# Kernel tuning notes

Measured on AMD Instinct MI355X. Metric: run time of the kernel, lower is better.

## Reference

```python
import jax, jax.numpy as jnp
from jax import lax
import numpy as np

HEADS = 8
DIM_HEAD = 64


def setup_inputs() -> dict:
    key = jax.random.key(0)
    ks = jax.random.split(key, 6)
    dim, inner = 256, HEADS * DIM_HEAD
    fmap = jax.random.normal(ks[0], (8, dim, 128, 128), dtype=jnp.float32)
    w_q = jax.random.normal(ks[1], (inner, dim), dtype=jnp.float32) * (dim ** -0.5)
    w_dw = jax.random.normal(ks[2], (dim, 1, 3, 3), dtype=jnp.float32) * (9 ** -0.5)
    w_pw = jax.random.normal(ks[3], (2 * inner, dim), dtype=jnp.float32) * (dim ** -0.5)
    w_out = jax.random.normal(ks[4], (dim, inner), dtype=jnp.float32) * (inner ** -0.5)
    b_out = jnp.zeros((dim,), dtype=jnp.float32)
    return {"fmap": fmap, "w_q": w_q, "w_dw": w_dw, "w_pw": w_pw, "w_out": w_out, "b_out": b_out}


def _linear_attention(fmap, w_q, w_dw, w_pw, w_out, b_out):
    B, C, H, W = fmap.shape
    h, d = HEADS, DIM_HEAD
    scale = d ** -0.5
    N = H * W
    # to_q: 1x1 conv, no bias
    q = jnp.einsum('bcxy,oc->boxy', fmap, w_q)  # [B, h*d, H, W]
    # to_kv: depthwise 3x3 (pad 1) then pointwise 1x1, no bias
    dw = lax.conv_general_dilated(
        fmap, w_dw, window_strides=(1, 1), padding=((1, 1), (1, 1)),
        dimension_numbers=('NCHW', 'OIHW', 'NCHW'), feature_group_count=C)
    kv = jnp.einsum('bcxy,oc->boxy', dw, w_pw)  # [B, 2*h*d, H, W]
    k, v = jnp.split(kv, 2, axis=1)

    def to_bhnc(t):  # b (h c) x y -> (b h) (x y) c
        return t.reshape(B, h, d, N).transpose(0, 1, 3, 2).reshape(B * h, N, d)

    q, k, v = to_bhnc(q), to_bhnc(k), to_bhnc(v)
    q = jax.nn.softmax(q, axis=-1) * scale  # softmax over feature dim
    k = jax.nn.softmax(k, axis=-2)          # softmax over spatial dim
    context = jnp.einsum('bnd,bne->bde', k, v)   # [(B*h), d, d]
    out = jnp.einsum('bnd,bde->bne', q, context)  # [(B*h), N, d]
    # (b h) (x y) d -> b (h d) x y
    out = out.reshape(B, h, N, d).transpose(0, 1, 3, 2).reshape(B, h * d, H, W)
    out = jax.nn.gelu(out, approximate=False)
    out = jnp.einsum('bcxy,oc->boxy', out, w_out) + b_out[None, :, None, None]
    return out


def reference(fmap, w_q, w_dw, w_pw, w_out, b_out):
    return _linear_attention(fmap, w_q, w_dw, w_pw, w_out, b_out)
```

## Files before the change

kernel.cpp:

```cpp
#include <hip/hip_runtime.h>
#include <math.h>

#define NPIX 16384

typedef __bf16 bf16x8 __attribute__((ext_vector_type(8)));
typedef float f32x4 __attribute__((ext_vector_type(4)));
typedef unsigned short u16;
typedef unsigned int u32;

__device__ __forceinline__ u16 f2bf(float f) {
    u32 u = __float_as_uint(f);
    u32 r = (u + 0x7FFFu + ((u >> 16) & 1u)) >> 16;
    return (u16)r;
}
__device__ __forceinline__ float bf2f(u32 s) { return __uint_as_float(s << 16); }
__device__ __forceinline__ u32 pk2(float a, float b) {
    return (u32)f2bf(a) | ((u32)f2bf(b) << 16);
}

__global__ __launch_bounds__(256) void k_cvtw(
    const float* __restrict__ wq, const float* __restrict__ wpw,
    const float* __restrict__ wout,
    u16* __restrict__ wq_b, u16* __restrict__ wpw_b, u16* __restrict__ wout_b)
{
    int id = (blockIdx.x * 256 + threadIdx.x) * 4;
    const float* s; u16* d; int off;
    if (id < 131072)      { s = wq;   d = wq_b;   off = id; }
    else if (id < 393216) { s = wpw;  d = wpw_b;  off = id - 131072; }
    else                  { s = wout; d = wout_b; off = id - 393216; }
    f32x4 v = *(const f32x4*)(s + off);
    uint2 u; u.x = pk2(v[0], v[1]); u.y = pk2(v[2], v[3]);
    *(uint2*)(d + off) = u;
}

__global__ __launch_bounds__(256) void k_conv(
    const float* __restrict__ fmap, const float* __restrict__ wdw,
    u16* __restrict__ fmapT, u16* __restrict__ dwT)
{
    const int t = threadIdx.x;
    const int lane = t & 63, w = t >> 6;
    const int x = blockIdx.x, b = blockIdx.y;

    __shared__ u16 dst[2][128][66];

    const float mLf = (lane == 0) ? 0.f : 1.f;
    const float mRf = (lane == 63) ? 0.f : 1.f;
    const float mTf = (x > 0) ? 1.f : 0.f;
    const float mBf = (x < 127) ? 1.f : 0.f;
    const int dT = (x > 0) ? -128 : 0;
    const int dB = (x < 127) ? 128 : 0;

    const size_t nbase = (size_t)b * NPIX + (size_t)x * 128;

    for (int chunk = 0; chunk < 4; ++chunk) {
        for (int g = 0; g < 4; ++g) {
            const int cl0 = w * 16 + g * 4;
            const int c0 = chunk * 64 + cl0;
            float2 T[4], M[4], B[4];
            #pragma unroll
            for (int i = 0; i < 4; ++i) {
                const float* p = fmap + ((size_t)(b * 256 + c0 + i)) * NPIX + (size_t)x * 128;
                M[i] = ((const float2*)p)[lane];
                T[i] = ((const float2*)(p + dT))[lane];
                B[i] = ((const float2*)(p + dB))[lane];
            }
            #pragma unroll
            for (int i = 0; i < 4; ++i) {
                const float* wc = wdw + (c0 + i) * 9;
                float w0 = wc[0] * mTf, w1 = wc[1] * mTf, w2 = wc[2] * mTf;
                float w3 = wc[3],       w4 = wc[4],       w5 = wc[5];
                float w6 = wc[6] * mBf, w7 = wc[7] * mBf, w8 = wc[8] * mBf;
                float tL = __shfl_up(T[i].y, 1) * mLf;
                float mL_ = __shfl_up(M[i].y, 1) * mLf;
                float bL = __shfl_up(B[i].y, 1) * mLf;
                float tR = __shfl_down(T[i].x, 1) * mRf;
                float mR_ = __shfl_down(M[i].x, 1) * mRf;
                float bR = __shfl_down(B[i].x, 1) * mRf;
                float o0 = w0 * tL     + w1 * T[i].x + w2 * T[i].y
                         + w3 * mL_    + w4 * M[i].x + w5 * M[i].y
                         + w6 * bL     + w7 * B[i].x + w8 * B[i].y;
                float o1 = w0 * T[i].x + w1 * T[i].y + w2 * tR
                         + w3 * M[i].x + w4 * M[i].y + w5 * mR_
                         + w6 * B[i].x + w7 * B[i].y + w8 * bR;
                int cl = cl0 + i;
                dst[0][2 * lane][cl]     = f2bf(M[i].x);
                dst[0][2 * lane + 1][cl] = f2bf(M[i].y);
                dst[1][2 * lane][cl]     = f2bf(o0);
                dst[1][2 * lane + 1][cl] = f2bf(o1);
            }
        }
        __syncthreads();
        #pragma unroll
        for (int T2 = 0; T2 < 2; ++T2) {
            u16* gp = T2 ? dwT : fmapT;
            #pragma unroll
            for (int it = 0; it < 4; ++it) {
                int u = it * 256 + t;
                int y = u >> 3, c8 = (u & 7) * 8;
                const u16* s = &dst[T2][y][c8];
                uint4 val;
                val.x = *(const u32*)(s);
                val.y = *(const u32*)(s + 2);
                val.z = *(const u32*)(s + 4);
                val.w = *(const u32*)(s + 6);
                *(uint4*)(gp + (nbase + y) * 256 + chunk * 64 + c8) = val;
            }
        }
        __syncthreads();
    }
}

__global__ __launch_bounds__(256, 2) void k_kvctx(
    const u16* __restrict__ dwT, const u16* __restrict__ wpw,
    float* __restrict__ ctx, float* __restrict__ denom)
{
    const int t = threadIdx.x;
    const int lane = t & 63, w = t >> 6;
    const int l15 = lane & 15, quad = lane >> 4;

    const int L = blockIdx.x;
    const int work = (L & 7) * 128 + (L >> 3);
    const int s = work >> 6;
    const int b = (work >> 3) & 7;
    const int h = work & 7;
    const int bh = b * 8 + h;

    __shared__ __align__(16) u16 sm[32768];
    u16* EL = sm;
    u16* VL = sm + 8192;

    const int ph = (w & 1) * 64;
    const int ck = (w >> 1);

    const int srow = t >> 3;
    const int sg = t & 7;

    f32x4 ctxacc[4] = {};
    float dpart[4] = {0.f, 0.f, 0.f, 0.f};

    uint4 ra[4], rb[4];

#define KV_STAGE_LOAD(stv, kcv)                                                        \
    {                                                                                  \
        const u16* xr = dwT + ((size_t)b * NPIX + s * 1024 + (stv) * 128) * 256;       \
        _Pragma("unroll")                                                              \
        for (int p = 0; p < 4; ++p) {                                                  \
            int row = srow + 32 * p;                                                   \
            int wr = (row < 64) ? (h * 64 + row) : (512 + h * 64 + (row - 64));        \
            ra[p] = *(const uint4*)(wpw + (size_t)wr * 256 + (kcv) * 64 + sg * 8);     \
            rb[p] = *(const uint4*)(xr + (size_t)row * 256 + (kcv) * 64 + sg * 8);     \
        }                                                                              \
    }

#define KV_STAGE_WRITE(bufi)                                                           \
    {                                                                                  \
        u16* Ad = sm + (bufi) * 8192;                                                  \
        u16* Bd = sm + 16384 + (bufi) * 8192;                                          \
        _Pragma("unroll")                                                              \
        for (int p = 0; p < 4; ++p) {                                                  \
            int row = srow + 32 * p;                                                   \
            int off = row * 64 + ((sg ^ (row & 7)) << 3);                              \
            *(uint4*)(Ad + off) = ra[p];                                               \
            *(uint4*)(Bd + off) = rb[p];                                               \
        }                                                                              \
    }

    KV_STAGE_LOAD(0, 0);

    for (int st = 0; st < 8; ++st) {
        KV_STAGE_WRITE(0);
        __syncthreads();
        f32x4 acc[4][4] = {};
        #pragma unroll
        for (int kc = 0; kc < 4; ++kc) {
            if (kc < 3) KV_STAGE_LOAD(st, kc + 1);
            {
                const u16* Ax = sm + (kc & 1) * 8192;
                const u16* Bx = sm + 16384 + (kc & 1) * 8192;
                #pragma unroll
                for (int kk = 0; kk < 64; kk += 32) {
                    bf16x8 av[4], bv[4];
                    #pragma unroll
                    for (int mf = 0; mf < 4; ++mf) {
                        int pr = ph + mf * 16 + l15;
                        int pg = ((kk >> 3) + quad) ^ (pr & 7);
                        av[mf] = *(const bf16x8*)(Bx + pr * 64 + (pg << 3));
                    }
                    #pragma unroll
                    for (int nf = 0; nf < 4; ++nf) {
                        int wr2 = ck * 64 + nf * 16 + l15;
                        int wg = ((kk >> 3) + quad) ^ (wr2 & 7);
                        bv[nf] = *(const bf16x8*)(Ax + wr2 * 64 + (wg << 3));
                    }
                    #pragma unroll
                    for (int mf = 0; mf < 4; ++mf)
                        #pragma unroll
                        for (int nf = 0; nf < 4; ++nf)
                            acc[mf][nf] = __builtin_amdgcn_mfma_f32_16x16x32_bf16(av[mf], bv[nf], acc[mf][nf], 0, 0, 0);
                }
            }
            if (kc < 3) {
                KV_STAGE_WRITE((kc + 1) & 1);
                __syncthreads();
            }
        }
        __syncthreads();
        u16* dst = ck ? VL : EL;
        #pragma unroll
        for (int nf = 0; nf < 4; ++nf) {
            const int ch = nf * 16 + l15;
            const int key = ch & 7;
            float colsum = 0.f;
            #pragma unroll
            for (int mf = 0; mf < 4; ++mf) {
                const int c = ph + mf * 16 + quad * 4;
                float v0 = acc[mf][nf][0], v1 = acc[mf][nf][1];
                float v2 = acc[mf][nf][2], v3 = acc[mf][nf][3];
                if (ck == 0) {
                    v0 = __expf(v0); v1 = __expf(v1);
                    v2 = __expf(v2); v3 = __expf(v3);
                    colsum += (v0 + v1) + (v2 + v3);
                }
                uint2 u; u.x = pk2(v0, v1); u.y = pk2(v2, v3);
                int addr = ch * 128 + ((((c >> 3) ^ key)) << 3) + (c & 7);
                *(uint2*)(dst + addr) = u;
            }
            if (ck == 0) {
                colsum += __shfl_xor(colsum, 16);
                colsum += __shfl_xor(colsum, 32);
                dpart[nf] += colsum;
            }
        }
        if (st < 7) KV_STAGE_LOAD(st + 1, 0);
        __syncthreads();
        #pragma unroll
        for (int kk2 = 0; kk2 < 128; kk2 += 32) {
            int ar = w * 16 + l15;
            int ag = ((kk2 >> 3) + quad) ^ (ar & 7);
            bf16x8 av = *(const bf16x8*)(VL + ar * 128 + (ag << 3));
            #pragma unroll
            for (int nf = 0; nf < 4; ++nf) {
                int br = nf * 16 + l15;
                int bg = ((kk2 >> 3) + quad) ^ (br & 7);
                bf16x8 bv = *(const bf16x8*)(EL + br * 128 + (bg << 3));
                ctxacc[nf] = __builtin_amdgcn_mfma_f32_16x16x32_bf16(av, bv, ctxacc[nf], 0, 0, 0);
            }
        }
        __syncthreads();
    }
    #pragma unroll
    for (int nf = 0; nf < 4; ++nf)
        #pragma unroll
        for (int r = 0; r < 4; ++r) {
            int e = w * 16 + quad * 4 + r;
            int d = nf * 16 + l15;
            atomicAdd(ctx + ((size_t)bh * 64 + e) * 64 + d, ctxacc[nf][r]);
        }
    if (ck == 0 && quad == 0) {
        #pragma unroll
        for (int nf = 0; nf < 4; ++nf)
            atomicAdd(denom + bh * 64 + nf * 16 + l15, dpart[nf]);
    }
#undef KV_STAGE_LOAD
#undef KV_STAGE_WRITE
}

__global__ __launch_bounds__(256) void k_proj_q(
    const u16* __restrict__ fmapT, const u16* __restrict__ wq,
    u16* __restrict__ q)
{
    const int t = threadIdx.x;
    const int lane = t & 63, w = t >> 6;
    const int l15 = lane & 15, quad = lane >> 4;
    const int n0 = blockIdx.x * 128;
    const int o0 = blockIdx.y * 128;
    const int b  = blockIdx.z;
    __shared__ __align__(16) unsigned char smraw[71680];
    u16* sm16 = (u16*)smraw;
    f32x4 acc[4][4] = {};
    const int mh = (w >> 1) * 64, nh = (w & 1) * 64;
    const u16* wrow = wq + (size_t)o0 * 256;
    const u16* xrow = fmapT + ((size_t)b * NPIX + n0) * 256;
    const int srow = t >> 3;
    const int sg = t & 7;
    uint4 ra[4], rb[4];

#define Q_STAGE_LOAD(kcv)                                                              \
    {                                                                                  \
        _Pragma("unroll")                                                              \
        for (int p = 0; p < 4; ++p) {                                                  \
            int row = srow + 32 * p;                                                   \
            ra[p] = *(const uint4*)(wrow + (size_t)row * 256 + (kcv) * 64 + sg * 8);   \
            rb[p] = *(const uint4*)(xrow + (size_t)row * 256 + (kcv) * 64 + sg * 8);   \
        }                                                                              \
    }

#define Q_STAGE_WRITE(bufi)                                                            \
    {                                                                                  \
        u16* Ad = sm16 + (bufi) * 8192;                                                \
        u16* Bd = sm16 + 16384 + (bufi) * 8192;                                        \
        _Pragma("unroll")                                                              \
        for (int p = 0; p < 4; ++p) {                                                  \
            int row = srow + 32 * p;                                                   \
            int off = row * 64 + ((sg ^ (row & 7)) << 3);                              \
            *(uint4*)(Ad + off) = ra[p];                                               \
            *(uint4*)(Bd + off) = rb[p];                                               \
        }                                                                              \
    }

    Q_STAGE_LOAD(0);
    Q_STAGE_WRITE(0);
    __syncthreads();
    #pragma unroll
    for (int kc = 0; kc < 4; ++kc) {
        if (kc < 3) Q_STAGE_LOAD(kc + 1);
        {
            const u16* Ax = sm16 + (kc & 1) * 8192;
            const u16* Bx = sm16 + 16384 + (kc & 1) * 8192;
            #pragma unroll
            for (int kk = 0; kk < 64; kk += 32) {
                bf16x8 av[4], bv[4];
                #pragma unroll
                for (int mf = 0; mf < 4; ++mf) {
                    int arow = mh + mf * 16 + l15;
                    int agr = ((kk >> 3) + quad) ^ (arow & 7);
                    av[mf] = *(const bf16x8*)(Ax + arow * 64 + (agr << 3));
                }
                #pragma unroll
                for (int nf = 0; nf < 4; ++nf) {
                    int brow = nh + nf * 16 + l15;
                    int bgr = ((kk >> 3) + quad) ^ (brow & 7);
                    bv[nf] = *(const bf16x8*)(Bx + brow * 64 + (bgr << 3));
                }
                #pragma unroll
                for (int mf = 0; mf < 4; ++mf)
                    #pragma unroll
                    for (int nf = 0; nf < 4; ++nf)
                        acc[mf][nf] = __builtin_amdgcn_mfma_f32_16x16x32_bf16(av[mf], bv[nf], acc[mf][nf], 0, 0, 0);
            }
        }
        if (kc < 3) {
            Q_STAGE_WRITE((kc + 1) & 1);
            __syncthreads();
        }
    }
    __syncthreads();
    float* ep = (float*)smraw;
    #pragma unroll
    for (int mf = 0; mf < 4; ++mf)
        #pragma unroll
        for (int nf = 0; nf < 4; ++nf)
            #pragma unroll
            for (int r = 0; r < 4; ++r) {
                int row = mh + mf * 16 + quad * 4 + r;
                int col = nh + nf * 16 + l15;
                ep[col * 140 + row] = acc[mf][nf][r];
            }
    __syncthreads();
    const int h0 = blockIdx.y * 2;
    for (int p = 0; p < 8; ++p) {
        int unit = p * 32 + (t >> 3);
        int pix = unit >> 1, hh = unit & 1;
        int d8 = (t & 7) * 8;
        f32x4 v0 = *(const f32x4*)(ep + pix * 140 + hh * 64 + d8);
        f32x4 v1 = *(const f32x4*)(ep + pix * 140 + hh * 64 + d8 + 4);
        float e0 = __expf(v0[0]), e1 = __expf(v0[1]), e2 = __expf(v0[2]), e3 = __expf(v0[3]);
        float e4 = __expf(v1[0]), e5 = __expf(v1[1]), e6 = __expf(v1[2]), e7 = __expf(v1[3]);
        float s = ((e0 + e1) + (e2 + e3)) + ((e4 + e5) + (e6 + e7));
        s += __shfl_xor(s, 1); s += __shfl_xor(s, 2); s += __shfl_xor(s, 4);
        float r = 0.125f / s;
        uint4 u;
        u.x = pk2(e0 * r, e1 * r); u.y = pk2(e2 * r, e3 * r);
        u.z = pk2(e4 * r, e5 * r); u.w = pk2(e6 * r, e7 * r);
        size_t off = (((size_t)b * 8 + h0 + hh) * NPIX + n0 + pix) * 64 + d8;
        *(uint4*)(q + off) = u;
    }
#undef Q_STAGE_LOAD
#undef Q_STAGE_WRITE
}

__global__ __launch_bounds__(256) void k_attnout(
    const u16* __restrict__ q, const float* __restrict__ ctx,
    const float* __restrict__ denom, const u16* __restrict__ wout,
    const float* __restrict__ bout, float* __restrict__ out)
{
    const int t = threadIdx.x;
    const int lane = t & 63, w = t >> 6;
    const int l15 = lane & 15, quad = lane >> 4;
    const int n0 = blockIdx.x * 32;
    const int b  = blockIdx.y;
    __shared__ __align__(16) u16 tmp[32 * 520];
    __shared__ __align__(16) unsigned char R[20480];
    u16* qs = (u16*)R;
    u16* cs = (u16*)(R + 4608);
    u16* ws = (u16*)R;
    for (int h = 0; h < 8; ++h) {
        __syncthreads();
        {
            int row = t >> 3, g = t & 7;
            *(uint4*)(qs + row * 72 + g * 8) =
                *(const uint4*)(q + (((size_t)b * 8 + h) * NPIX + n0 + row) * 64 + g * 8);
        }
        const int bh = b * 8 + h;
        #pragma unroll
        for (int p = 0; p < 4; ++p) {
            int idx = p * 256 + t;
            int e = idx >> 4, dq = (idx & 15) * 4;
            f32x4 c4 = *(const f32x4*)(ctx + ((size_t)bh * 64 + e) * 64 + dq);
            f32x4 d4 = *(const f32x4*)(denom + bh * 64 + dq);
            uint2 u;
            u.x = pk2(c4[0] / d4[0], c4[1] / d4[1]);
            u.y = pk2(c4[2] / d4[2], c4[3] / d4[3]);
            *(uint2*)(cs + e * 72 + dq) = u;
        }
        __syncthreads();
        f32x4 a1[2] = {};
        #pragma unroll
        for (int kk = 0; kk < 64; kk += 32) {
            bf16x8 av = *(const bf16x8*)(qs + ((w & 1) * 16 + l15) * 72 + kk + quad * 8);
            #pragma unroll
            for (int j = 0; j < 2; ++j) {
                int nf = (w >> 1) * 2 + j;
                bf16x8 bv = *(const bf16x8*)(cs + (nf * 16 + l15) * 72 + kk + quad * 8);
                a1[j] = __builtin_amdgcn_mfma_f32_16x16x32_bf16(av, bv, a1[j], 0, 0, 0);
            }
        }
        #pragma unroll
        for (int j = 0; j < 2; ++j)
            #pragma unroll
            for (int r = 0; r < 4; ++r) {
                int pix = (w & 1) * 16 + quad * 4 + r;
                int e = ((w >> 1) * 2 + j) * 16 + l15;
                float x = a1[j][r];
                float gel = 0.5f * x * (1.0f + erff(x * 0.70710678118654752f));
                tmp[pix * 520 + h * 64 + e] = f2bf(gel);
            }
    }
    __syncthreads();
    f32x4 acc[4][2] = {};
    for (int kc = 0; kc < 16; ++kc) {
        __syncthreads();
        #pragma unroll
        for (int p = 0; p < 4; ++p) {
            int c = (t >> 2) + 64 * p, g = t & 3;
            *(uint4*)(ws + c * 40 + g * 8) = *(const uint4*)(wout + (size_t)c * 512 + kc * 32 + g * 8);
        }
        __syncthreads();
        bf16x8 av[4], bv[2];
        #pragma unroll
        for (int mf = 0; mf < 4; ++mf)
            av[mf] = *(const bf16x8*)(ws + (w * 64 + mf * 16 + l15) * 40 + quad * 8);
        #pragma unroll
        for (int nf = 0; nf < 2; ++nf)
            bv[nf] = *(const bf16x8*)(tmp + (nf * 16 + l15) * 520 + kc * 32 + quad * 8);
        #pragma unroll
        for (int mf = 0; mf < 4; ++mf)
            #pragma unroll
            for (int nf = 0; nf < 2; ++nf)
                acc[mf][nf] = __builtin_amdgcn_mfma_f32_16x16x32_bf16(av[mf], bv[nf], acc[mf][nf], 0, 0, 0);
    }
    #pragma unroll
    for (int mf = 0; mf < 4; ++mf)
        #pragma unroll
        for (int nf = 0; nf < 2; ++nf)
            #pragma unroll
            for (int r = 0; r < 4; ++r) {
                int c = w * 64 + mf * 16 + quad * 4 + r;
                int pix = nf * 16 + l15;
                out[((size_t)b * 256 + c) * NPIX + n0 + pix] = acc[mf][nf][r] + bout[c];
            }
}

extern "C" void kernel_launch(void* const* d_in, const int* in_sizes, int n_in,
                              void* d_out, int out_size, void* d_ws, size_t ws_size,
                              hipStream_t stream)
{
    const float* fmap  = (const float*)d_in[0];
    const float* w_q   = (const float*)d_in[1];
    const float* w_dw  = (const float*)d_in[2];
    const float* w_pw  = (const float*)d_in[3];
    const float* w_out = (const float*)d_in[4];
    const float* b_out = (const float*)d_in[5];
    float* out = (float*)d_out;
    char* ws = (char*)d_ws;

    u16* dwT     = (u16*)(ws);
    u16* fmapT   = (u16*)(ws + 67108864);
    u16* q       = (u16*)(ws + 134217728);
    float* ctx   = (float*)(ws + 402653184);
    float* denom = (float*)(ws + 403701760);
    u16* wq_b    = (u16*)(ws + 403718144);
    u16* wpw_b   = (u16*)(ws + 403980288);
    u16* wout_b  = (u16*)(ws + 404504576);

    hipMemsetAsync(ws + 402653184, 0, 1048576 + 16384, stream);
    k_cvtw<<<512, 256, 0, stream>>>(w_q, w_pw, w_out, wq_b, wpw_b, wout_b);
    k_conv<<<dim3(128, 8), 256, 0, stream>>>(fmap, w_dw, fmapT, dwT);
    k_kvctx<<<1024, 256, 0, stream>>>(dwT, wpw_b, ctx, denom);
    k_proj_q<<<dim3(128, 4, 8), 256, 0, stream>>>(fmapT, wq_b, q);
    k_attnout<<<dim3(512, 8), 256, 0, stream>>>(q, ctx, denom, wout_b, b_out, out);
}
```

Before: 735.3 us.

## Precompute normalized bf16 context and pipeline per-head attnout with output projection

Adds a small kernel that divides the context by the denominator once and stores it as bf16, so each attnout block no longer redoes that fp32 division per head. The attnout kernel now handles 64 pixels per block and folds the output projection into the head loop, accumulating in registers instead of staging all heads in a 32x520 shared buffer. Loads for the next head (q, context, and the matching w_out slice) are prefetched into registers while the current head's MMAs run. This costs an extra launch, more registers and more shared memory, and w_out is reloaded per head per block.

```diff
diff --git a/kernel.cpp b/kernel.cpp
--- a/kernel.cpp
+++ b/kernel.cpp
@@ -265,6 +265,27 @@
 #undef KV_STAGE_WRITE
 }
 
+__global__ __launch_bounds__(256) void k_ctxn(
+    const float* __restrict__ ctx, const float* __restrict__ denom,
+    u16* __restrict__ ctxn)
+{
+    const int bh = blockIdx.x;
+    const int t = threadIdx.x;
+    const int e = t >> 2, d0 = (t & 3) * 16;
+    const float* cr = ctx + ((size_t)bh * 64 + e) * 64 + d0;
+    const float* dr = denom + bh * 64 + d0;
+    u16* o = ctxn + ((size_t)bh * 64 + e) * 64 + d0;
+    #pragma unroll
+    for (int i = 0; i < 4; ++i) {
+        f32x4 c = *(const f32x4*)(cr + i * 4);
+        f32x4 dv = *(const f32x4*)(dr + i * 4);
+        uint2 u;
+        u.x = pk2(c[0] / dv[0], c[1] / dv[1]);
+        u.y = pk2(c[2] / dv[2], c[3] / dv[3]);
+        *(uint2*)(o + i * 4) = u;
+    }
+}
+
 __global__ __launch_bounds__(256) void k_proj_q(
     const u16* __restrict__ fmapT, const u16* __restrict__ wq,
     u16* __restrict__ q)
@@ -380,94 +401,113 @@
 }
 
 __global__ __launch_bounds__(256) void k_attnout(
-    const u16* __restrict__ q, const float* __restrict__ ctx,
-    const float* __restrict__ denom, const u16* __restrict__ wout,
-    const float* __restrict__ bout, float* __restrict__ out)
+    const u16* __restrict__ q, const u16* __restrict__ ctxn,
+    const u16* __restrict__ wout, const float* __restrict__ bout,
+    float* __restrict__ out)
 {
     const int t = threadIdx.x;
     const int lane = t & 63, w = t >> 6;
     const int l15 = lane & 15, quad = lane >> 4;
-    const int n0 = blockIdx.x * 32;
+    const int n0 = blockIdx.x * 64;
     const int b  = blockIdx.y;
-    __shared__ __align__(16) u16 tmp[32 * 520];
-    __shared__ __align__(16) unsigned char R[20480];
-    u16* qs = (u16*)R;
-    u16* cs = (u16*)(R + 4608);
-    u16* ws = (u16*)R;
+
+    __shared__ __align__(16) u16 qs[64 * 72];
+    __shared__ __align__(16) u16 cs[64 * 72];
+    __shared__ __align__(16) u16 G [64 * 72];
+    __shared__ __align__(16) u16 WS[256 * 72];
+
+    uint4 rq[2], rc[2], rw[8];
+
+    auto LOADH = [&](int h) {
+        const u16* qb = q + (((size_t)(b * 8 + h)) * NPIX + n0) * 64;
+        const u16* cb = ctxn + ((size_t)(b * 8 + h)) * 64 * 64;
+        #pragma unroll
+        for (int p = 0; p < 2; ++p) {
+            int i = p * 256 + t; int row = i >> 3, g = i & 7;
+            rq[p] = *(const uint4*)(qb + row * 64 + g * 8);
+            rc[p] = *(const uint4*)(cb + row * 64 + g * 8);
+        }
+        #pragma unroll
+        for (int p = 0; p < 8; ++p) {
+            int i = p * 256 + t; int row = i >> 3, g = i & 7;
+            rw[p] = *(const uint4*)(wout + (size_t)row * 512 + h * 64 + g * 8);
+        }
+    };
+    auto WRITEH = [&]() {
+        #pragma unroll
+        for (int p = 0; p < 2; ++p) {
+            int i = p * 256 + t; int row = i >> 3, g = i & 7;
+            *(uint4*)(qs + row * 72 + g * 8) = rq[p];
+            *(uint4*)(cs + row * 72 + g * 8) = rc[p];
+        }
+        #pragma unroll
+        for (int p = 0; p < 8; ++p) {
+            int i = p * 256 + t; int row = i >> 3, g = i & 7;
+            *(uint4*)(WS + row * 72 + g * 8) = rw[p];
+        }
+    };
+
+    f32x4 acc[4][4] = {};
+
+    LOADH(0);
+    WRITEH();
+    __syncthreads();
+
     for (int h = 0; h < 8; ++h) {
-        __syncthreads();
-        {
-            int row = t >> 3, g = t & 7;
-            *(uint4*)(qs + row * 72 + g * 8) =
-                *(const uint4*)(q + (((size_t)b * 8 + h) * NPIX + n0 + row) * 64 + g * 8);
-        }
-        const int bh = b * 8 + h;
-        #pragma unroll
-        for (int p = 0; p < 4; ++p) {
-            int idx = p * 256 + t;
-            int e = idx >> 4, dq = (idx & 15) * 4;
-            f32x4 c4 = *(const f32x4*)(ctx + ((size_t)bh * 64 + e) * 64 + dq);
-            f32x4 d4 = *(const f32x4*)(denom + bh * 64 + dq);
-            uint2 u;
-            u.x = pk2(c4[0] / d4[0], c4[1] / d4[1]);
-            u.y = pk2(c4[2] / d4[2], c4[3] / d4[3]);
-            *(uint2*)(cs + e * 72 + dq) = u;
-        }
-        __syncthreads();
-        f32x4 a1[2] = {};
+        f32x4 a1[4] = {};
         #pragma unroll
         for (int kk = 0; kk < 64; kk += 32) {
-            bf16x8 av = *(const bf16x8*)(qs + ((w & 1) * 16 + l15) * 72 + kk + quad * 8);
-            #pragma unroll
-            for (int j = 0; j < 2; ++j) {
-                int nf = (w >> 1) * 2 + j;
-                bf16x8 bv = *(const bf16x8*)(cs + (nf * 16 + l15) * 72 + kk + quad * 8);
-                a1[j] = __builtin_amdgcn_mfma_f32_16x16x32_bf16(av, bv, a1[j], 0, 0, 0);
-            }
-        }
-        #pragma unroll
-        for (int j = 0; j < 2; ++j)
-            #pragma unroll
-            for (int r = 0; r < 4; ++r) {
-                int pix = (w & 1) * 16 + quad * 4 + r;
-                int e = ((w >> 1) * 2 + j) * 16 + l15;
-                float x = a1[j][r];
-                float gel = 0.5f * x * (1.0f + erff(x * 0.70710678118654752f));
-                tmp[pix * 520 + h * 64 + e] = f2bf(gel);
-            }
-    }
-    __syncthreads();
-    f32x4 acc[4][2] = {};
-    for (int kc = 0; kc < 16; ++kc) {
-        __syncthreads();
-        #pragma unroll
-        for (int p = 0; p < 4; ++p) {
-            int c = (t >> 2) + 64 * p, g = t & 3;
-            *(uint4*)(ws + c * 40 + g * 8) = *(const uint4*)(wout + (size_t)c * 512 + kc * 32 + g * 8);
-        }
-        __syncthreads();
-        bf16x8 av[4], bv[2];
-        #pragma unroll
-        for (int mf = 0; mf < 4; ++mf)
-            av[mf] = *(const bf16x8*)(ws + (w * 64 + mf * 16 + l15) * 40 + quad * 8);
-        #pragma unroll
-        for (int nf = 0; nf < 2; ++nf)
-            bv[nf] = *(const bf16x8*)(tmp + (nf * 16 + l15) * 520 + kc * 32 + quad * 8);
-        #pragma unroll
-        for (int mf = 0; mf < 4; ++mf)
-            #pragma unroll
-            for (int nf = 0; nf < 2; ++nf)
-                acc[mf][nf] = __builtin_amdgcn_mfma_f32_16x16x32_bf16(av[mf], bv[nf], acc[mf][nf], 0, 0, 0);
+            bf16x8 av = *(const bf16x8*)(cs + (w * 16 + l15) * 72 + kk + quad * 8);
+            #pragma unroll
+            for (int nf = 0; nf < 4; ++nf) {
+                bf16x8 bv = *(const bf16x8*)(qs + (nf * 16 + l15) * 72 + kk + quad * 8);
+                a1[nf] = __builtin_amdgcn_mfma_f32_16x16x32_bf16(av, bv, a1[nf], 0, 0, 0);
+            }
+        }
+        #pragma unroll
+        for (int nf = 0; nf < 4; ++nf) {
+            int px = nf * 16 + l15;
+            int e0 = w * 16 + quad * 4;
+            float x0 = a1[nf][0], x1 = a1[nf][1], x2 = a1[nf][2], x3 = a1[nf][3];
+            x0 = 0.5f * x0 * (1.0f + erff(x0 * 0.70710678118654752f));
+            x1 = 0.5f * x1 * (1.0f + erff(x1 * 0.70710678118654752f));
+            x2 = 0.5f * x2 * (1.0f + erff(x2 * 0.70710678118654752f));
+            x3 = 0.5f * x3 * (1.0f + erff(x3 * 0.70710678118654752f));
+            uint2 u; u.x = pk2(x0, x1); u.y = pk2(x2, x3);
+            *(uint2*)(G + px * 72 + e0) = u;
+        }
+        __syncthreads();
+        if (h < 7) LOADH(h + 1);
+        #pragma unroll
+        for (int kk = 0; kk < 64; kk += 32) {
+            bf16x8 av2[4], bv2[4];
+            #pragma unroll
+            for (int mf = 0; mf < 4; ++mf)
+                av2[mf] = *(const bf16x8*)(WS + (w * 64 + mf * 16 + l15) * 72 + kk + quad * 8);
+            #pragma unroll
+            for (int nf = 0; nf < 4; ++nf)
+                bv2[nf] = *(const bf16x8*)(G + (nf * 16 + l15) * 72 + kk + quad * 8);
+            #pragma unroll
+            for (int mf = 0; mf < 4; ++mf)
+                #pragma unroll
+                for (int nf = 0; nf < 4; ++nf)
+                    acc[mf][nf] = __builtin_amdgcn_mfma_f32_16x16x32_bf16(av2[mf], bv2[nf], acc[mf][nf], 0, 0, 0);
+        }
+        __syncthreads();
+        if (h < 7) {
+            WRITEH();
+            __syncthreads();
+        }
     }
     #pragma unroll
     for (int mf = 0; mf < 4; ++mf)
         #pragma unroll
-        for (int nf = 0; nf < 2; ++nf)
+        for (int nf = 0; nf < 4; ++nf)
             #pragma unroll
             for (int r = 0; r < 4; ++r) {
                 int c = w * 64 + mf * 16 + quad * 4 + r;
-                int pix = nf * 16 + l15;
-                out[((size_t)b * 256 + c) * NPIX + n0 + pix] = acc[mf][nf][r] + bout[c];
+                int px = nf * 16 + l15;
+                out[((size_t)b * 256 + c) * NPIX + n0 + px] = acc[mf][nf][r] + bout[c];
             }
 }
 
@@ -485,6 +525,7 @@
     char* ws = (char*)d_ws;
 
     u16* dwT     = (u16*)(ws);
+    u16* ctxn    = (u16*)(ws);
     u16* fmapT   = (u16*)(ws + 67108864);
     u16* q       = (u16*)(ws + 134217728);
     float* ctx   = (float*)(ws + 402653184);
@@ -497,6 +538,7 @@
     k_cvtw<<<512, 256, 0, stream>>>(w_q, w_pw, w_out, wq_b, wpw_b, wout_b);
     k_conv<<<dim3(128, 8), 256, 0, stream>>>(fmap, w_dw, fmapT, dwT);
     k_kvctx<<<1024, 256, 0, stream>>>(dwT, wpw_b, ctx, denom);
+    k_ctxn<<<64, 256, 0, stream>>>(ctx, denom, ctxn);
     k_proj_q<<<dim3(128, 4, 8), 256, 0, stream>>>(fmapT, wq_b, q);
-    k_attnout<<<dim3(512, 8), 256, 0, stream>>>(q, ctx, denom, wout_b, b_out, out);
-}
+    k_attnout<<<dim3(256, 8), 256, 0, stream>>>(q, ctxn, wout_b, b_out, out);
+}
```

Result: slower. 842.9 us (+14.6%).

## Fuse q@context and GELU into q projection; split output projection kernel

Applied to the files above, without the earlier changes.

Context normalisation moves into a small pre-pass that writes a bf16 normalised context. The q-projection kernel then applies the feature softmax in registers and multiplies by the context with MFMA, applying GELU and writing G directly. This removes the separate q round trip and the per-block context reload in the old attention-output kernel. The output projection becomes a simpler kernel with a 128-pixel tile that reads G and w_out straight from global memory without LDS staging, which may raise register pressure and global-load traffic.

```diff
diff --git a/kernel.cpp b/kernel.cpp
--- a/kernel.cpp
+++ b/kernel.cpp
@@ -265,9 +265,30 @@
 #undef KV_STAGE_WRITE
 }
 
-__global__ __launch_bounds__(256) void k_proj_q(
+__global__ __launch_bounds__(256) void k_ctxn(
+    const float* __restrict__ ctx, const float* __restrict__ denom,
+    u16* __restrict__ ctxn)
+{
+    const int bh = blockIdx.x;
+    const int t = threadIdx.x;
+    const int e = t >> 2, d0 = (t & 3) * 16;
+    const float* cr = ctx + ((size_t)bh * 64 + e) * 64 + d0;
+    const float* dr = denom + bh * 64 + d0;
+    u16* o = ctxn + ((size_t)bh * 64 + e) * 64 + d0;
+    #pragma unroll
+    for (int i = 0; i < 4; ++i) {
+        f32x4 c = *(const f32x4*)(cr + i * 4);
+        f32x4 dv = *(const f32x4*)(dr + i * 4);
+        uint2 u;
+        u.x = pk2(c[0] / dv[0], c[1] / dv[1]);
+        u.y = pk2(c[2] / dv[2], c[3] / dv[3]);
+        *(uint2*)(o + i * 4) = u;
+    }
+}
+
+__global__ __launch_bounds__(256) void k_qattn(
     const u16* __restrict__ fmapT, const u16* __restrict__ wq,
-    u16* __restrict__ q)
+    const u16* __restrict__ ctxn, u16* __restrict__ G)
 {
     const int t = threadIdx.x;
     const int lane = t & 63, w = t >> 6;
@@ -357,118 +378,117 @@
                 ep[col * 140 + row] = acc[mf][nf][r];
             }
     __syncthreads();
-    const int h0 = blockIdx.y * 2;
-    for (int p = 0; p < 8; ++p) {
-        int unit = p * 32 + (t >> 3);
-        int pix = unit >> 1, hh = unit & 1;
-        int d8 = (t & 7) * 8;
-        f32x4 v0 = *(const f32x4*)(ep + pix * 140 + hh * 64 + d8);
-        f32x4 v1 = *(const f32x4*)(ep + pix * 140 + hh * 64 + d8 + 4);
-        float e0 = __expf(v0[0]), e1 = __expf(v0[1]), e2 = __expf(v0[2]), e3 = __expf(v0[3]);
-        float e4 = __expf(v1[0]), e5 = __expf(v1[1]), e6 = __expf(v1[2]), e7 = __expf(v1[3]);
-        float s = ((e0 + e1) + (e2 + e3)) + ((e4 + e5) + (e6 + e7));
-        s += __shfl_xor(s, 1); s += __shfl_xor(s, 2); s += __shfl_xor(s, 4);
-        float r = 0.125f / s;
-        uint4 u;
-        u.x = pk2(e0 * r, e1 * r); u.y = pk2(e2 * r, e3 * r);
-        u.z = pk2(e4 * r, e5 * r); u.w = pk2(e6 * r, e7 * r);
-        size_t off = (((size_t)b * 8 + h0 + hh) * NPIX + n0 + pix) * 64 + d8;
-        *(uint4*)(q + off) = u;
+
+    const int hh = w >> 1;
+    const int pxh = (w & 1) * 64;
+    const int bh = b * 8 + blockIdx.y * 2 + hh;
+    const u16* cb = ctxn + (size_t)bh * 64 * 64;
+    u16* Gb = G + ((size_t)bh * NPIX + n0) * 64;
+
+    bf16x8 pa[4][2];
+    #pragma unroll
+    for (int mf = 0; mf < 4; ++mf) {
+        int px = pxh + mf * 16 + l15;
+        const float* src = ep + px * 140 + hh * 64 + quad * 8;
+        f32x4 u0 = *(const f32x4*)(src);
+        f32x4 u1 = *(const f32x4*)(src + 4);
+        f32x4 u2 = *(const f32x4*)(src + 32);
+        f32x4 u3 = *(const f32x4*)(src + 36);
+        float x0 = __expf(u0[0]), x1 = __expf(u0[1]), x2 = __expf(u0[2]), x3 = __expf(u0[3]);
+        float x4 = __expf(u1[0]), x5 = __expf(u1[1]), x6 = __expf(u1[2]), x7 = __expf(u1[3]);
+        float y0 = __expf(u2[0]), y1 = __expf(u2[1]), y2 = __expf(u2[2]), y3 = __expf(u2[3]);
+        float y4 = __expf(u3[0]), y5 = __expf(u3[1]), y6 = __expf(u3[2]), y7 = __expf(u3[3]);
+        float s8 = (((x0 + x1) + (x2 + x3)) + ((x4 + x5) + (x6 + x7)))
+                 + (((y0 + y1) + (y2 + y3)) + ((y4 + y5) + (y6 + y7)));
+        s8 += __shfl_xor(s8, 16);
+        s8 += __shfl_xor(s8, 32);
+        float rs = 0.125f / s8;
+        union { u32 uw[4]; bf16x8 v; } pka, pkb;
+        pka.uw[0] = pk2(x0 * rs, x1 * rs); pka.uw[1] = pk2(x2 * rs, x3 * rs);
+        pka.uw[2] = pk2(x4 * rs, x5 * rs); pka.uw[3] = pk2(x6 * rs, x7 * rs);
+        pkb.uw[0] = pk2(y0 * rs, y1 * rs); pkb.uw[1] = pk2(y2 * rs, y3 * rs);
+        pkb.uw[2] = pk2(y4 * rs, y5 * rs); pkb.uw[3] = pk2(y6 * rs, y7 * rs);
+        pa[mf][0] = pka.v;
+        pa[mf][1] = pkb.v;
+    }
+
+    f32x4 a2[4][4] = {};
+    #pragma unroll
+    for (int j = 0; j < 2; ++j) {
+        bf16x8 cav[4];
+        #pragma unroll
+        for (int mfE = 0; mfE < 4; ++mfE)
+            cav[mfE] = *(const bf16x8*)(cb + (size_t)(mfE * 16 + l15) * 64 + j * 32 + quad * 8);
+        #pragma unroll
+        for (int mfE = 0; mfE < 4; ++mfE)
+            #pragma unroll
+            for (int nfP = 0; nfP < 4; ++nfP)
+                a2[mfE][nfP] = __builtin_amdgcn_mfma_f32_16x16x32_bf16(cav[mfE], pa[nfP][j], a2[mfE][nfP], 0, 0, 0);
+    }
+
+    #pragma unroll
+    for (int nfP = 0; nfP < 4; ++nfP) {
+        int px = pxh + nfP * 16 + l15;
+        u16* gp = Gb + (size_t)px * 64;
+        #pragma unroll
+        for (int mfE = 0; mfE < 4; ++mfE) {
+            int e0 = mfE * 16 + quad * 4;
+            float g0 = a2[mfE][nfP][0], g1 = a2[mfE][nfP][1];
+            float g2 = a2[mfE][nfP][2], g3 = a2[mfE][nfP][3];
+            g0 = 0.5f * g0 * (1.0f + erff(g0 * 0.70710678118654752f));
+            g1 = 0.5f * g1 * (1.0f + erff(g1 * 0.70710678118654752f));
+            g2 = 0.5f * g2 * (1.0f + erff(g2 * 0.70710678118654752f));
+            g3 = 0.5f * g3 * (1.0f + erff(g3 * 0.70710678118654752f));
+            uint2 u; u.x = pk2(g0, g1); u.y = pk2(g2, g3);
+            *(uint2*)(gp + e0) = u;
+        }
     }
 #undef Q_STAGE_LOAD
 #undef Q_STAGE_WRITE
 }
 
-__global__ __launch_bounds__(256) void k_attnout(
-    const u16* __restrict__ q, const float* __restrict__ ctx,
-    const float* __restrict__ denom, const u16* __restrict__ wout,
+__global__ __launch_bounds__(256) void k_out(
+    const u16* __restrict__ G, const u16* __restrict__ wout,
     const float* __restrict__ bout, float* __restrict__ out)
 {
     const int t = threadIdx.x;
     const int lane = t & 63, w = t >> 6;
     const int l15 = lane & 15, quad = lane >> 4;
-    const int n0 = blockIdx.x * 32;
+    const int n0 = blockIdx.x * 128;
     const int b  = blockIdx.y;
-    __shared__ __align__(16) u16 tmp[32 * 520];
-    __shared__ __align__(16) unsigned char R[20480];
-    u16* qs = (u16*)R;
-    u16* cs = (u16*)(R + 4608);
-    u16* ws = (u16*)R;
+
+    f32x4 acc[8][4] = {};
     for (int h = 0; h < 8; ++h) {
-        __syncthreads();
-        {
-            int row = t >> 3, g = t & 7;
-            *(uint4*)(qs + row * 72 + g * 8) =
-                *(const uint4*)(q + (((size_t)b * 8 + h) * NPIX + n0 + row) * 64 + g * 8);
-        }
-        const int bh = b * 8 + h;
-        #pragma unroll
-        for (int p = 0; p < 4; ++p) {
-            int idx = p * 256 + t;
-            int e = idx >> 4, dq = (idx & 15) * 4;
-            f32x4 c4 = *(const f32x4*)(ctx + ((size_t)bh * 64 + e) * 64 + dq);
-            f32x4 d4 = *(const f32x4*)(denom + bh * 64 + dq);
-            uint2 u;
-            u.x = pk2(c4[0] / d4[0], c4[1] / d4[1]);
-            u.y = pk2(c4[2] / d4[2], c4[3] / d4[3]);
-            *(uint2*)(cs + e * 72 + dq) = u;
-        }
-        __syncthreads();
-        f32x4 a1[2] = {};
-        #pragma unroll
-        for (int kk = 0; kk < 64; kk += 32) {
-            bf16x8 av = *(const bf16x8*)(qs + ((w & 1) * 16 + l15) * 72 + kk + quad * 8);
-            #pragma unroll
-            for (int j = 0; j < 2; ++j) {
-                int nf = (w >> 1) * 2 + j;
-                bf16x8 bv = *(const bf16x8*)(cs + (nf * 16 + l15) * 72 + kk + quad * 8);
-                a1[j] = __builtin_amdgcn_mfma_f32_16x16x32_bf16(av, bv, a1[j], 0, 0, 0);
-            }
-        }
-        #pragma unroll
-        for (int j = 0; j < 2; ++j)
-            #pragma unroll
-            for (int r = 0; r < 4; ++r) {
-                int pix = (w & 1) * 16 + quad * 4 + r;
-                int e = ((w >> 1) * 2 + j) * 16 + l15;
-                float x = a1[j][r];
-                float gel = 0.5f * x * (1.0f + erff(x * 0.70710678118654752f));
-                tmp[pix * 520 + h * 64 + e] = f2bf(gel);
-            }
-    }
-    __syncthreads();
-    f32x4 acc[4][2] = {};
-    for (int kc = 0; kc < 16; ++kc) {
-        __syncthreads();
-        #pragma unroll
-        for (int p = 0; p < 4; ++p) {
-            int c = (t >> 2) + 64 * p, g = t & 3;
-            *(uint4*)(ws + c * 40 + g * 8) = *(const uint4*)(wout + (size_t)c * 512 + kc * 32 + g * 8);
-        }
-        __syncthreads();
-        bf16x8 av[4], bv[2];
-        #pragma unroll
-        for (int mf = 0; mf < 4; ++mf)
-            av[mf] = *(const bf16x8*)(ws + (w * 64 + mf * 16 + l15) * 40 + quad * 8);
-        #pragma unroll
-        for (int nf = 0; nf < 2; ++nf)
-            bv[nf] = *(const bf16x8*)(tmp + (nf * 16 + l15) * 520 + kc * 32 + quad * 8);
-        #pragma unroll
-        for (int mf = 0; mf < 4; ++mf)
-            #pragma unroll
-            for (int nf = 0; nf < 2; ++nf)
-                acc[mf][nf] = __builtin_amdgcn_mfma_f32_16x16x32_bf16(av[mf], bv[nf], acc[mf][nf], 0, 0, 0);
-    }
-    #pragma unroll
-    for (int mf = 0; mf < 4; ++mf)
-        #pragma unroll
-        for (int nf = 0; nf < 2; ++nf)
-            #pragma unroll
-            for (int r = 0; r < 4; ++r) {
-                int c = w * 64 + mf * 16 + quad * 4 + r;
-                int pix = nf * 16 + l15;
-                out[((size_t)b * 256 + c) * NPIX + n0 + pix] = acc[mf][nf][r] + bout[c];
-            }
+        const u16* Gh = G + (((size_t)(b * 8 + h)) * NPIX + n0) * 64;
+        #pragma unroll
+        for (int j = 0; j < 2; ++j) {
+            bf16x8 av[8], bv[4];
+            #pragma unroll
+            for (int mfP = 0; mfP < 8; ++mfP)
+                av[mfP] = *(const bf16x8*)(Gh + (size_t)(mfP * 16 + l15) * 64 + j * 32 + quad * 8);
+            #pragma unroll
+            for (int nfC = 0; nfC < 4; ++nfC)
+                bv[nfC] = *(const bf16x8*)(wout + (size_t)(w * 64 + nfC * 16 + l15) * 512 + h * 64 + j * 32 + quad * 8);
+            #pragma unroll
+            for (int mfP = 0; mfP < 8; ++mfP)
+                #pragma unroll
+                for (int nfC = 0; nfC < 4; ++nfC)
+                    acc[mfP][nfC] = __builtin_amdgcn_mfma_f32_16x16x32_bf16(av[mfP], bv[nfC], acc[mfP][nfC], 0, 0, 0);
+        }
+    }
+    #pragma unroll
+    for (int nfC = 0; nfC < 4; ++nfC) {
+        int ch = w * 64 + nfC * 16 + l15;
+        float bb = bout[ch];
+        float* orow = out + ((size_t)b * 256 + ch) * NPIX + n0;
+        #pragma unroll
+        for (int mfP = 0; mfP < 8; ++mfP) {
+            int px0 = mfP * 16 + quad * 4;
+            f32x4 v = acc[mfP][nfC];
+            v[0] += bb; v[1] += bb; v[2] += bb; v[3] += bb;
+            *(f32x4*)(orow + px0) = v;
+        }
+    }
 }
 
 extern "C" void kernel_launch(void* const* d_in, const int* in_sizes, int n_in,
@@ -485,8 +505,9 @@
     char* ws = (char*)d_ws;
 
     u16* dwT     = (u16*)(ws);
+    u16* ctxn    = (u16*)(ws);
     u16* fmapT   = (u16*)(ws + 67108864);
-    u16* q       = (u16*)(ws + 134217728);
+    u16* G       = (u16*)(ws + 134217728);
     float* ctx   = (float*)(ws + 402653184);
     float* denom = (float*)(ws + 403701760);
     u16* wq_b    = (u16*)(ws + 403718144);
@@ -497,6 +518,7 @@
     k_cvtw<<<512, 256, 0, stream>>>(w_q, w_pw, w_out, wq_b, wpw_b, wout_b);
     k_conv<<<dim3(128, 8), 256, 0, stream>>>(fmap, w_dw, fmapT, dwT);
     k_kvctx<<<1024, 256, 0, stream>>>(dwT, wpw_b, ctx, denom);
-    k_proj_q<<<dim3(128, 4, 8), 256, 0, stream>>>(fmapT, wq_b, q);
-    k_attnout<<<dim3(512, 8), 256, 0, stream>>>(q, ctx, denom, wout_b, b_out, out);
-}
+    k_ctxn<<<64, 256, 0, stream>>>(ctx, denom, ctxn);
+    k_qattn<<<dim3(128, 4, 8), 256, 0, stream>>>(fmapT, wq_b, ctxn, G);
+    k_out<<<dim3(128, 8), 256, 0, stream>>>(G, wout_b, b_out, out);
+}
```

New measurement: 751.6 us. 1.02x slower.
